# Optimization experiments

Hardware: AMD Instinct MI355X
Metric: run time of the kernel (lower is better)

Reference implementation:

```python
import jax, jax.numpy as jnp
import numpy as np

T, B, S = 2000, 64, 128   # seq_len, batch, alphabet_len
W = 16                    # beam_width
BLANK = 0                 # blank_index
PRUNE = 0.001             # prune_threshold
NONBLANK = np.array([c for c in range(S) if c != BLANK], dtype=np.int32)  # [S-1]
HASH_MULT = np.uint32(1000003)


def setup_inputs() -> dict:
    key = jax.random.key(0)
    k1, k2 = jax.random.split(key)
    x = jax.random.uniform(k1, (T, B, S), dtype=jnp.float32)
    lengths = jax.random.randint(k2, (B,), T // 2, T + 1, dtype=jnp.int32)
    return {"x": x, "lengths": lengths}


def _decode_one(ctc, length):
    # ctc: [T, S] probabilities for one utterance; length: scalar int32.
    nonblank = jnp.asarray(NONBLANK)
    arW = jnp.arange(W)

    prefixes0 = -jnp.ones((W, T), jnp.int32)          # padded prefixes
    len0 = jnp.zeros((W,), jnp.int32)
    # beam 0 = empty prefix (hash 0); others get unique sentinel hashes, prob 0
    hash0 = jnp.where(arW == 0, jnp.uint32(0),
                      jnp.uint32(0x80000000) + arW.astype(jnp.uint32))
    pb0 = jnp.zeros((W,), jnp.float32).at[0].set(1.0)  # Pb[-1][()] = 1
    pnb0 = jnp.zeros((W,), jnp.float32)                # Pnb[-1][()] = 0

    def step(carry, xs):
        prefixes, plen, h, p_b, p_nb = carry
        probs_raw, t = xs
        # pruning: symbols with prob <= threshold contribute nothing
        probs = jnp.where(probs_raw > PRUNE, probs_raw, 0.0)
        p_tot = p_b + p_nb
        last = jnp.where(plen > 0, prefixes[arW, jnp.maximum(plen - 1, 0)], -1)

        # --- candidates 0..W-1: prefix unchanged ---
        c0_pb = probs[BLANK] * p_tot                              # blank extends
        c0_pnb = jnp.where(last >= 0, probs[last] * p_nb, 0.0)    # repeat-last

        # --- candidates for beam b extended by nonblank symbol c: [W, S-1] ---
        pc = probs[nonblank]                                      # [S-1]
        rep = nonblank[None, :] == last[:, None]                  # [W, S-1]
        e_pnb = pc[None, :] * jnp.where(rep, p_b[:, None], p_tot[:, None])
        e_h = h[:, None] * HASH_MULT + (nonblank.astype(jnp.uint32) + 1)[None, :]
        e_pnb_f = e_pnb.reshape(-1)                               # [W*(S-1)]
        e_h_f = e_h.reshape(-1)

        # Merge: an extension can only coincide with another beam's unchanged
        # prefix (extensions of distinct prefixes are always distinct).
        eq = h[:, None] == e_h_f[None, :]                         # [W, W*(S-1)]
        u_pnb = c0_pnb + eq.astype(jnp.float32) @ e_pnb_f
        u_pb = c0_pb
        dup = eq.any(axis=0)

        key = jnp.concatenate([u_pb + u_pnb, jnp.where(dup, -1.0, e_pnb_f)])
        cand_pb = jnp.concatenate([u_pb, jnp.zeros_like(e_pnb_f)])
        cand_pnb = jnp.concatenate([u_pnb, jnp.where(dup, 0.0, e_pnb_f)])
        cand_h = jnp.concatenate([h, e_h_f])
        _, idx = jax.lax.top_k(key, W)

        ext = idx >= W
        q = jnp.maximum(idx - W, 0)
        nb = jnp.where(ext, q // (S - 1), idx)                    # source beam
        csym = jnp.where(ext, nonblank[q % (S - 1)], -1)          # appended sym
        base_pref = prefixes[nb]
        base_len = plen[nb]
        pos = jnp.arange(T)[None, :]
        n_pref = jnp.where((csym[:, None] >= 0) & (pos == base_len[:, None]),
                           csym[:, None], base_pref)
        n_len = base_len + (csym >= 0).astype(jnp.int32)
        n_h = cand_h[idx]
        n_pb = cand_pb[idx]
        n_pnb = cand_pnb[idx]

        # rescale to avoid fp underflow over long sequences (ranking-preserving;
        # the torch module returns only the argmax prefix, not raw scores)
        scale = 1.0 / jnp.maximum(jnp.max(n_pb + n_pnb), 1e-30)
        n_pb = n_pb * scale
        n_pnb = n_pnb * scale

        valid = t < length
        new = (n_pref, n_len, n_h, n_pb, n_pnb)
        old = (prefixes, plen, h, p_b, p_nb)
        carry = tuple(jnp.where(valid, a, b) for a, b in zip(new, old))
        return carry, None

    carry, _ = jax.lax.scan(jax.checkpoint(step),
                            (prefixes0, len0, hash0, pb0, pnb0),
                            (ctc, jnp.arange(T, dtype=jnp.int32)))
    prefixes, plen, _, p_b, p_nb = carry
    # top_k already sorted beams descending by total prob -> beam 0 is best
    return prefixes[0], plen[0], p_b[0] + p_nb[0]


def reference(x, lengths):
    # x: [T, B, S]; lengths: [B] int32
    prefs, lens, scores = jax.vmap(_decode_one, in_axes=(1, 0))(x, lengths)
    # prefs: [B, T] best prefix per element, padded with -1; lens: [B]
    return prefs, lens, scores
```

## Files before the change

kernel.cpp:

```cpp
#include <hip/hip_runtime.h>
#include <stdint.h>

#define T_ 2000
#define B_ 64
#define S_ 128
#define HASHM 1000003u

typedef float f4 __attribute__((ext_vector_type(4)));
typedef int i2v __attribute__((ext_vector_type(2)));

#if defined(__has_builtin)
#if __has_builtin(__builtin_amdgcn_permlane32_swap)
#define HAVE_PL32 1
#endif
#if __has_builtin(__builtin_amdgcn_permlane16_swap)
#define HAVE_PL16 1
#endif
#endif

__device__ __forceinline__ uint32_t rl(uint32_t v, int ln) {
  return (uint32_t)__builtin_amdgcn_readlane((int)v, ln);
}
__device__ __forceinline__ float rlf(float v, int ln) {
  return __uint_as_float(rl(__float_as_uint(v), ln));
}

__device__ __forceinline__ uint32_t fkey(float v) {
  uint32_t b = __float_as_uint(v);
  return b ^ (((int32_t)b < 0) ? 0xFFFFFFFFu : 0x80000000u);
}

__device__ __forceinline__ void wave_lds_fence() {
  asm volatile("s_waitcnt lgkmcnt(0)" ::: "memory");
}

template<int J>
__device__ __forceinline__ uint32_t bfly_u32(uint32_t v) {
  if constexpr (J == 1)
    return (uint32_t)__builtin_amdgcn_update_dpp((int)v, (int)v, 0xB1, 0xF, 0xF, false);
  else if constexpr (J == 2)
    return (uint32_t)__builtin_amdgcn_update_dpp((int)v, (int)v, 0x4E, 0xF, 0xF, false);
  else if constexpr (J == 4) {
    uint32_t a = (uint32_t)__builtin_amdgcn_update_dpp((int)v, (int)v, 0x12C, 0xF, 0xF, false);
    uint32_t b = (uint32_t)__builtin_amdgcn_update_dpp((int)v, (int)v, 0x124, 0xF, 0xF, false);
    return ((threadIdx.x & 4) == 0) ? a : b;
  } else if constexpr (J == 8)
    return (uint32_t)__builtin_amdgcn_update_dpp((int)v, (int)v, 0x128, 0xF, 0xF, false);
  else if constexpr (J == 16) {
#ifdef HAVE_PL16
    i2v r = __builtin_amdgcn_permlane16_swap((int)v, (int)v, false, false);
    return (uint32_t)(((threadIdx.x & 16) == 0) ? r[1] : r[0]);
#else
    return (uint32_t)__builtin_amdgcn_ds_swizzle((int)v, 0x401F);
#endif
  } else {
#ifdef HAVE_PL32
    i2v r = __builtin_amdgcn_permlane32_swap((int)v, (int)v, false, false);
    return (uint32_t)(((threadIdx.x & 32) == 0) ? r[1] : r[0]);
#else
    return (uint32_t)__shfl_xor((int)v, 32);
#endif
  }
}
template<int J>
__device__ __forceinline__ uint64_t bfly_u64(uint64_t v) {
  uint32_t lo = bfly_u32<J>((uint32_t)v);
  uint32_t hi = bfly_u32<J>((uint32_t)(v >> 32));
  return ((uint64_t)hi << 32) | lo;
}

#define BSTF(KK, J) { float p_ = __uint_as_float(bfly_u32<J>(__float_as_uint(v))); \
  bool d_ = ((ln & (KK)) == 0) == ((ln & (J)) == 0); \
  float mx_ = fmaxf(v, p_), mn_ = fminf(v, p_); v = d_ ? mx_ : mn_; }
#define BST64(KK, J) { uint64_t p_ = bfly_u64<J>(v); \
  bool d_ = ((ln & (KK)) == 0) == ((ln & (J)) == 0); \
  uint64_t mx_ = v > p_ ? v : p_, mn_ = v > p_ ? p_ : v; v = d_ ? mx_ : mn_; }

__device__ __forceinline__ float bsort64_f32(float v, const int ln) {
  BSTF(2, 1)
  BSTF(4, 2) BSTF(4, 1)
  BSTF(8, 4) BSTF(8, 2) BSTF(8, 1)
  BSTF(16, 8) BSTF(16, 4) BSTF(16, 2) BSTF(16, 1)
  BSTF(32, 16) BSTF(32, 8) BSTF(32, 4) BSTF(32, 2) BSTF(32, 1)
  BSTF(64, 32) BSTF(64, 16) BSTF(64, 8) BSTF(64, 4) BSTF(64, 2) BSTF(64, 1)
  return v;
}

template<int WIDTH>
__device__ __forceinline__ uint64_t bsortN_u64(uint64_t v, const int ln) {
  BST64(2, 1)
  BST64(4, 2) BST64(4, 1)
  BST64(8, 4) BST64(8, 2) BST64(8, 1)
  BST64(16, 8) BST64(16, 4) BST64(16, 2) BST64(16, 1)
  if constexpr (WIDTH >= 32) {
    BST64(32, 16) BST64(32, 8) BST64(32, 4) BST64(32, 2) BST64(32, 1)
  }
  if constexpr (WIDTH >= 64) {
    BST64(64, 32) BST64(64, 16) BST64(64, 8) BST64(64, 4) BST64(64, 2) BST64(64, 1)
  }
  return v;
}

__device__ __forceinline__ uint32_t incl_scan_add(uint32_t v) {
  v += (uint32_t)__builtin_amdgcn_update_dpp(0, (int)v, 0x111, 0xF, 0xF, false);
  v += (uint32_t)__builtin_amdgcn_update_dpp(0, (int)v, 0x112, 0xF, 0xF, false);
  v += (uint32_t)__builtin_amdgcn_update_dpp(0, (int)v, 0x114, 0xF, 0xF, false);
  v += (uint32_t)__builtin_amdgcn_update_dpp(0, (int)v, 0x118, 0xF, 0xF, false);
  v += (uint32_t)__builtin_amdgcn_update_dpp(0, (int)v, 0x142, 0xA, 0xF, false);
  v += (uint32_t)__builtin_amdgcn_update_dpp(0, (int)v, 0x143, 0xC, 0xF, false);
  return v;
}

template<int CTRL>
__device__ __forceinline__ uint64_t dpp_max_u64(uint64_t v) {
  uint32_t lo = (uint32_t)v, hi = (uint32_t)(v >> 32);
  uint32_t slo = (uint32_t)__builtin_amdgcn_update_dpp(0, (int)lo, CTRL, 0xF, 0xF, false);
  uint32_t shi = (uint32_t)__builtin_amdgcn_update_dpp(0, (int)hi, CTRL, 0xF, 0xF, false);
  uint64_t o = ((uint64_t)shi << 32) | slo;
  return (o > v) ? o : v;
}
__device__ __forceinline__ uint64_t wave_max_u64(uint64_t v) {
  v = dpp_max_u64<0x111>(v);
  v = dpp_max_u64<0x112>(v);
  v = dpp_max_u64<0x114>(v);
  v = dpp_max_u64<0x118>(v);
  v = dpp_max_u64<0x142>(v);
  v = dpp_max_u64<0x143>(v);
  uint32_t lo = rl((uint32_t)v, 63);
  uint32_t hi = rl((uint32_t)(v >> 32), 63);
  return ((uint64_t)hi << 32) | lo;
}

__global__ __launch_bounds__(64, 1) void ctc_decode_kernel(
    const float* __restrict__ x, const int* __restrict__ lengths,
    float* __restrict__ out) {
  __shared__ uint64_t surv[64];
  __shared__ __align__(16) float Pr[2][S_];
  __shared__ __align__(8) uint16_t trace[T_ * 16];

  const int b = blockIdx.x;
  const int lane = (int)threadIdx.x;
  const int m = lane & 15;
  const int g = lane >> 4;
  const int lenb = lengths[b];

  uint32_t h = (m == 0) ? 0u : (0x80000000u + (uint32_t)m);
  float pb = (m == 0) ? 1.0f : 0.0f;
  float pnb = 0.0f;
  int last = -1;
  int len = 0;

  float cur0;
  {
    const float* xt = x + (size_t)b * S_;
    float a0 = xt[lane], a1 = xt[lane + 64];
    float p0 = (a0 > 0.001f) ? a0 : 0.0f;
    float p1 = (a1 > 0.001f) ? a1 : 0.0f;
    Pr[0][lane] = p0;
    Pr[0][lane + 64] = p1;
    cur0 = p0;
  }

  const uint32_t cbase = 1u + 32u * (uint32_t)g;
  const uint32_t nrefb = ~(15u + (uint32_t)m * 127u + 32u * (uint32_t)g);

  for (int t = 0; t < lenb; ++t) {
    const float* P = Pr[t & 1];
    float r0n = 0.0f, r1n = 0.0f;
    const bool hasNext = (t + 1 < lenb);
    if (hasNext) {
      const float* xt = x + ((size_t)(t + 1) * B_ + b) * S_;
      r0n = xt[lane];
      r1n = xt[lane + 64];
    }
    wave_lds_fence();
    const uint32_t hM = h * HASHM;
    const uint32_t hMc = hM + cbase;

    const float ptot = __fadd_rn(pb, pnb);
    const float P0 = rlf(cur0, 0);
    const float c0pb = __fmul_rn(P0, ptot);
    const float plast = P[(last >= 0) ? last : 0];
    const float c0pnb = (last >= 0) ? __fmul_rn(plast, pnb) : 0.0f;

    uint32_t lmask = 0;
    uint32_t matchcnt = 0, jm = 0, cc = 1;
    #pragma unroll
    for (int j = 0; j < 16; ++j) {
      uint32_t s_h = rl(h, j);
      uint32_t p = s_h - hMc;
      lmask |= (p < 32u) ? (1u << (p & 31u)) : 0u;
      uint32_t d = h - s_h * HASHM;
      bool match = (d - 2u) <= 126u;
      cc = match ? (d - 1u) : cc;
      jm = match ? (uint32_t)j : jm;
      matchcnt += match ? 1u : 0u;
    }

    float term0;
    if (__builtin_expect(__ballot(matchcnt > 1u) == 0ull, 1)) {
      float tpb = __shfl(pb, (int)jm);
      float tpt = __shfl(ptot, (int)jm);
      int tlast = __shfl(last, (int)jm);
      float tv = P[cc];
      float sel = ((int)cc == tlast) ? tpb : tpt;
      term0 = (matchcnt != 0u) ? __fmul_rn(tv, sel) : 0.0f;
    } else {
      float term[16];
      #pragma unroll
      for (int j = 0; j < 16; ++j) {
        uint32_t s_h = rl(h, j);
        uint32_t d = h - s_h * HASHM;
        bool match2 = (d - 2u) <= 126u;
        uint32_t cc2 = match2 ? (d - 1u) : 1u;
        float tv = P[cc2];
        uint32_t slst = rl((uint32_t)last, j);
        float sel = (cc2 == slst) ? rlf(pb, j) : rlf(ptot, j);
        term[j] = match2 ? __fmul_rn(tv, sel) : 0.0f;
      }
      #pragma unroll
      for (int st = 1; st < 16; st <<= 1) {
        #pragma unroll
        for (int i2 = 0; i2 < 16; i2 += 2 * st)
          term[i2] = __fadd_rn(term[i2], term[i2 + st]);
      }
      term0 = term[0];
    }
    const float upnb = __fadd_rn(c0pnb, term0);
    const float key16 = __fadd_rn(c0pb, upnb);

    f4 pv[8];
    {
      const f4* P4 = (const f4*)(P + 32 * g);
      #pragma unroll
      for (int i = 0; i < 8; ++i) pv[i] = P4[i];
    }
    const int lk = last - 32 * g;
    float kf[32];
    #pragma unroll
    for (int k = 0; k < 32; ++k) {
      float pc = pv[k >> 2][k & 3];
      float sel = (k == lk) ? pb : ptot;
      float val = __fmul_rn(pc, sel);
      bool dup = (lmask >> k) & 1u;
      float kv = dup ? -1.0f : val;
      if (k == 0) kv = (lane < 16) ? key16 : kv;
      kf[k] = kv;
    }

    float mx[16];
    #pragma unroll
    for (int i = 0; i < 16; ++i) mx[i] = fmaxf(kf[2 * i], kf[2 * i + 1]);
    #pragma unroll
    for (int w2 = 8; w2 >= 1; w2 >>= 1) {
      #pragma unroll
      for (int i = 0; i < w2; ++i) mx[i] = fmaxf(mx[i], mx[i + w2]);
    }
    const float m1 = mx[0];

    float th = rlf(bsort64_f32(m1, lane), 15);

    uint32_t gcnt[4];
    #pragma unroll
    for (int grp = 0; grp < 4; ++grp) {
      uint32_t c2 = 0;
      #pragma unroll
      for (int k = grp * 8; k < grp * 8 + 8; ++k) c2 += (kf[k] >= th) ? 1u : 0u;
      gcnt[grp] = c2;
    }
    uint32_t cnt = (gcnt[0] + gcnt[1]) + (gcnt[2] + gcnt[3]);
    uint32_t incl = incl_scan_add(cnt);
    uint32_t M = rl(incl, 63);

    if (__builtin_expect(M > 64u, 0)) {
      float t1[16], t2[16];
      #pragma unroll
      for (int i = 0; i < 16; ++i) {
        float a2 = kf[2 * i], b2 = kf[2 * i + 1];
        t1[i] = fmaxf(a2, b2);
        t2[i] = fminf(a2, b2);
      }
      #pragma unroll
      for (int w2 = 8; w2 >= 1; w2 >>= 1) {
        #pragma unroll
        for (int i = 0; i < w2; ++i) {
          float A = t1[i], Bv = t1[i + w2];
          float sa = t2[i], sb = t2[i + w2];
          t1[i] = fmaxf(A, Bv);
          t2[i] = fmaxf(fminf(A, Bv), fmaxf(sa, sb));
        }
      }
      float th2 = rlf(bsort64_f32(t2[0], lane), 7);
      th = fmaxf(th, th2);
      #pragma unroll
      for (int grp = 0; grp < 4; ++grp) {
        uint32_t c2 = 0;
        #pragma unroll
        for (int k = grp * 8; k < grp * 8 + 8; ++k) c2 += (kf[k] >= th) ? 1u : 0u;
        gcnt[grp] = c2;
      }
      cnt = (gcnt[0] + gcnt[1]) + (gcnt[2] + gcnt[3]);
      incl = incl_scan_add(cnt);
      M = rl(incl, 63);
    }

    uint64_t selpk;
    if (__builtin_expect(M <= 64u, 1)) {
      uint64_t* dump = (uint64_t*)(&trace[(size_t)t * 16]);
      uint32_t base0 = incl - cnt;
      uint32_t base1 = base0 + gcnt[0];
      uint32_t base2 = base1 + gcnt[1];
      uint32_t base3 = base2 + gcnt[2];
      uint32_t bases[4] = {base0, base1, base2, base3};
      #pragma unroll
      for (int grp = 0; grp < 4; ++grp) {
        uint32_t pos = bases[grp];
        #pragma unroll
        for (int kk = 0; kk < 8; ++kk) {
          int k = grp * 8 + kk;
          bool q = kf[k] >= th;
          uint32_t nr = nrefb - (uint32_t)k;
          if (k == 0) nr = (lane < 16) ? ~(uint32_t)m : nr;
          uint64_t pk = ((uint64_t)__float_as_uint(kf[k]) << 32) | nr;
          uint64_t* dst = q ? &surv[pos] : dump;
          *dst = pk;
          pos += q ? 1u : 0u;
        }
      }
      wave_lds_fence();
      uint64_t w = ((uint32_t)lane < M) ? surv[lane] : 0ull;
      if (M <= 16u)      w = bsortN_u64<16>(w, lane);
      else if (M <= 32u) w = bsortN_u64<32>(w, lane);
      else               w = bsortN_u64<64>(w, lane);
      uint64_t s16 = bfly_u64<16>(w);
      uint64_t w01 = ((lane & 16) == 0) ? w : s16;
      uint64_t s32 = bfly_u64<32>(w01);
      selpk = ((lane & 32) == 0) ? w01 : s32;
    } else {
      uint32_t alive = 0xFFFFFFFFu;
      selpk = 0;
      #pragma unroll 1
      for (int r = 0; r < 16; ++r) {
        float bk = -1.0f;
        uint32_t bi = 0;
        #pragma unroll
        for (int k = 0; k < 32; ++k) {
          float kv = ((alive >> k) & 1u) ? kf[k] : -1.0f;
          if (kv > bk) { bk = kv; bi = (uint32_t)k; }
        }
        uint32_t nr = nrefb - bi;
        nr = (bi == 0u && lane < 16) ? ~(uint32_t)m : nr;
        uint64_t cand = ((uint64_t)fkey(bk) << 32) | nr;
        uint64_t win = wave_max_u64(cand);
        if (cand == win) alive &= ~(1u << bi);
        if (r == m) selpk = win;
      }
      uint32_t kb = (uint32_t)(selpk >> 32);
      kb ^= ((int32_t)kb < 0) ? 0x80000000u : 0xFFFFFFFFu;
      selpk = ((uint64_t)kb << 32) | (uint32_t)selpk;
    }

    if (hasNext) {
      float p0 = (r0n > 0.001f) ? r0n : 0.0f;
      float p1 = (r1n > 0.001f) ? r1n : 0.0f;
      float* Pn = Pr[(t + 1) & 1];
      Pn[lane] = p0;
      Pn[lane + 64] = p1;
      cur0 = p0;
    }

    const uint32_t gref = ~((uint32_t)selpk);
    const uint32_t keyw = (uint32_t)(selpk >> 32);
    const bool unch = gref < 16u;
    const uint32_t qq = gref - 16u;
    const uint32_t bsrc = qq / 127u;
    const uint32_t jj = qq - bsrc * 127u;
    const uint32_t c = jj + 1u;
    const int srcl = unch ? (int)gref : (int)bsrc;

    const uint32_t s_h = (uint32_t)__shfl((int)h, srcl);
    const uint32_t lpack = ((uint32_t)(last + 1) & 0xFFu) | ((uint32_t)len << 8);
    const uint32_t s_lp = (uint32_t)__shfl((int)lpack, srcl);
    const float s_upb = __shfl(c0pb, srcl);
    const float s_upn = __shfl(upnb, srcl);
    const int s_lst = (int)(s_lp & 0xFFu) - 1;
    const int s_len = (int)(s_lp >> 8);

    const uint32_t n_h = unch ? s_h : (s_h * HASHM + (jj + 2u));
    const float n_pb = unch ? s_upb : 0.0f;
    const float n_pnb = unch ? s_upn : __uint_as_float(keyw);
    const int n_last = unch ? s_lst : (int)c;
    const int n_len = unch ? s_len : (s_len + 1);

    if (lane < 16) {
      trace[t * 16 + lane] =
          (uint16_t)(((uint32_t)srcl << 8) | (unch ? 0u : c));
    }

    const float mxf = fmaxf(__uint_as_float(rl(keyw, 0)), 1e-30f);
    const float scale = __fdiv_rn(1.0f, mxf);
    pb = __fmul_rn(n_pb, scale);
    pnb = __fmul_rn(n_pnb, scale);
    h = n_h; last = n_last; len = n_len;
  }

  __syncthreads();

  float* prefs = out;
  float* lensOut = out + (B_ * T_);
  float* scores = out + (B_ * T_) + B_;

  const int L0 = __shfl(len, 0);
  for (int i = L0 + lane; i < T_; i += 64) prefs[(size_t)b * T_ + i] = -1.0f;

  if (lane == 0) {
    lensOut[b] = (float)L0;
    scores[b] = __fadd_rn(pb, pnb);
    int w = 0;
    int pos2 = L0 - 1;
    for (int t2 = lenb - 1; t2 >= 0; --t2) {
      uint32_t rec = trace[t2 * 16 + w];
      uint32_t sym = rec & 0xFFu;
      if (sym) { prefs[(size_t)b * T_ + pos2] = (float)sym; --pos2; }
      w = (int)(rec >> 8);
    }
  }
}

extern "C" void kernel_launch(void* const* d_in, const int* in_sizes, int n_in,
                              void* d_out, int out_size, void* d_ws, size_t ws_size,
                              hipStream_t stream) {
  (void)in_sizes; (void)n_in; (void)d_ws; (void)ws_size; (void)out_size;
  const float* x = (const float*)d_in[0];
  const int* lengths = (const int*)d_in[1];
  float* out = (float*)d_out;
  ctc_decode_kernel<<<B_, 64, 0, stream>>>(x, lengths, out);
}
```

Before: 7.241 ms.

## Shorten per-step critical path: single LDS buffer, no fences, reorder scoring

Drops the explicit LDS waitcnt fences and the double-buffered probability array, relying on in-order LDS access within a single wave. The unchanged-prefix merge term is moved after the threshold sort, and the rescale factor is taken from the sorted maximum earlier so it leaves the dependency chain. Candidate IDs now use a 128 stride, so divide-by-127 becomes shift/mask. The 64-bit bitonic compares use double fmax/fmin instead of integer compares. The risks are that removing the fences permits LDS reordering hazards, and that the double comparison misorders keys whose bit patterns are not valid ordered doubles.

After: 7.550 ms. 1.04x slower.

```diff
diff --git a/kernel.cpp b/kernel.cpp
--- a/kernel.cpp
+++ b/kernel.cpp
@@ -28,10 +28,6 @@
 __device__ __forceinline__ uint32_t fkey(float v) {
   uint32_t b = __float_as_uint(v);
   return b ^ (((int32_t)b < 0) ? 0xFFFFFFFFu : 0x80000000u);
-}
-
-__device__ __forceinline__ void wave_lds_fence() {
-  asm volatile("s_waitcnt lgkmcnt(0)" ::: "memory");
 }
 
 template<int J>
@@ -72,9 +68,13 @@
 #define BSTF(KK, J) { float p_ = __uint_as_float(bfly_u32<J>(__float_as_uint(v))); \
   bool d_ = ((ln & (KK)) == 0) == ((ln & (J)) == 0); \
   float mx_ = fmaxf(v, p_), mn_ = fminf(v, p_); v = d_ ? mx_ : mn_; }
+
 #define BST64(KK, J) { uint64_t p_ = bfly_u64<J>(v); \
   bool d_ = ((ln & (KK)) == 0) == ((ln & (J)) == 0); \
-  uint64_t mx_ = v > p_ ? v : p_, mn_ = v > p_ ? p_ : v; v = d_ ? mx_ : mn_; }
+  double vd_ = __longlong_as_double((long long)v); \
+  double pd_ = __longlong_as_double((long long)p_); \
+  double mx_ = fmax(vd_, pd_), mn_ = fmin(vd_, pd_); \
+  v = (uint64_t)__double_as_longlong(d_ ? mx_ : mn_); }
 
 __device__ __forceinline__ float bsort64_f32(float v, const int ln) {
   BSTF(2, 1)
@@ -135,7 +135,7 @@
     const float* __restrict__ x, const int* __restrict__ lengths,
     float* __restrict__ out) {
   __shared__ uint64_t surv[64];
-  __shared__ __align__(16) float Pr[2][S_];
+  __shared__ __align__(16) float Pr[S_];
   __shared__ __align__(8) uint16_t trace[T_ * 16];
 
   const int b = blockIdx.x;
@@ -156,16 +156,16 @@
     float a0 = xt[lane], a1 = xt[lane + 64];
     float p0 = (a0 > 0.001f) ? a0 : 0.0f;
     float p1 = (a1 > 0.001f) ? a1 : 0.0f;
-    Pr[0][lane] = p0;
-    Pr[0][lane + 64] = p1;
+    Pr[lane] = p0;
+    Pr[lane + 64] = p1;
     cur0 = p0;
   }
 
   const uint32_t cbase = 1u + 32u * (uint32_t)g;
-  const uint32_t nrefb = ~(15u + (uint32_t)m * 127u + 32u * (uint32_t)g);
+  const uint32_t nrefb = ~(15u + ((uint32_t)m << 7) + 32u * (uint32_t)g);
 
   for (int t = 0; t < lenb; ++t) {
-    const float* P = Pr[t & 1];
+    const float* P = Pr;
     float r0n = 0.0f, r1n = 0.0f;
     const bool hasNext = (t + 1 < lenb);
     if (hasNext) {
@@ -173,7 +173,6 @@
       r0n = xt[lane];
       r1n = xt[lane + 64];
     }
-    wave_lds_fence();
     const uint32_t hM = h * HASHM;
     const uint32_t hMc = hM + cbase;
 
@@ -181,7 +180,13 @@
     const float P0 = rlf(cur0, 0);
     const float c0pb = __fmul_rn(P0, ptot);
     const float plast = P[(last >= 0) ? last : 0];
-    const float c0pnb = (last >= 0) ? __fmul_rn(plast, pnb) : 0.0f;
+
+    f4 pv[8];
+    {
+      const f4* P4 = (const f4*)(P + 32 * g);
+      #pragma unroll
+      for (int i = 0; i < 8; ++i) pv[i] = P4[i];
+    }
 
     uint32_t lmask = 0;
     uint32_t matchcnt = 0, jm = 0, cc = 1;
@@ -196,45 +201,13 @@
       jm = match ? (uint32_t)j : jm;
       matchcnt += match ? 1u : 0u;
     }
-
-    float term0;
-    if (__builtin_expect(__ballot(matchcnt > 1u) == 0ull, 1)) {
-      float tpb = __shfl(pb, (int)jm);
-      float tpt = __shfl(ptot, (int)jm);
-      int tlast = __shfl(last, (int)jm);
-      float tv = P[cc];
-      float sel = ((int)cc == tlast) ? tpb : tpt;
-      term0 = (matchcnt != 0u) ? __fmul_rn(tv, sel) : 0.0f;
-    } else {
-      float term[16];
-      #pragma unroll
-      for (int j = 0; j < 16; ++j) {
-        uint32_t s_h = rl(h, j);
-        uint32_t d = h - s_h * HASHM;
-        bool match2 = (d - 2u) <= 126u;
-        uint32_t cc2 = match2 ? (d - 1u) : 1u;
-        float tv = P[cc2];
-        uint32_t slst = rl((uint32_t)last, j);
-        float sel = (cc2 == slst) ? rlf(pb, j) : rlf(ptot, j);
-        term[j] = match2 ? __fmul_rn(tv, sel) : 0.0f;
-      }
-      #pragma unroll
-      for (int st = 1; st < 16; st <<= 1) {
-        #pragma unroll
-        for (int i2 = 0; i2 < 16; i2 += 2 * st)
-          term[i2] = __fadd_rn(term[i2], term[i2 + st]);
-      }
-      term0 = term[0];
-    }
-    const float upnb = __fadd_rn(c0pnb, term0);
-    const float key16 = __fadd_rn(c0pb, upnb);
-
-    f4 pv[8];
-    {
-      const f4* P4 = (const f4*)(P + 32 * g);
-      #pragma unroll
-      for (int i = 0; i < 8; ++i) pv[i] = P4[i];
-    }
+    const bool multi = (__ballot(matchcnt > 1u) != 0ull);
+
+    float tv = P[cc];
+    float tpb = __shfl(pb, (int)jm);
+    float tpt = __shfl(ptot, (int)jm);
+    int tlast = __shfl(last, (int)jm);
+
     const int lk = last - 32 * g;
     float kf[32];
     #pragma unroll
@@ -244,7 +217,7 @@
       float val = __fmul_rn(pc, sel);
       bool dup = (lmask >> k) & 1u;
       float kv = dup ? -1.0f : val;
-      if (k == 0) kv = (lane < 16) ? key16 : kv;
+      if (k == 0) kv = (lane < 16) ? c0pb : kv;
       kf[k] = kv;
     }
 
@@ -256,9 +229,38 @@
       #pragma unroll
       for (int i = 0; i < w2; ++i) mx[i] = fmaxf(mx[i], mx[i + w2]);
     }
-    const float m1 = mx[0];
-
-    float th = rlf(bsort64_f32(m1, lane), 15);
+
+    float th = rlf(bsort64_f32(mx[0], lane), 15);
+
+    const float c0pnb = (last >= 0) ? __fmul_rn(plast, pnb) : 0.0f;
+    float term0;
+    if (__builtin_expect(!multi, 1)) {
+      float sel = ((int)cc == tlast) ? tpb : tpt;
+      term0 = (matchcnt != 0u) ? __fmul_rn(tv, sel) : 0.0f;
+    } else {
+      float term[16];
+      #pragma unroll
+      for (int j = 0; j < 16; ++j) {
+        uint32_t s_h = rl(h, j);
+        uint32_t d = h - s_h * HASHM;
+        bool match2 = (d - 2u) <= 126u;
+        uint32_t cc2 = match2 ? (d - 1u) : 1u;
+        float tv2 = P[cc2];
+        uint32_t slst = rl((uint32_t)last, j);
+        float sel = (cc2 == slst) ? rlf(pb, j) : rlf(ptot, j);
+        term[j] = match2 ? __fmul_rn(tv2, sel) : 0.0f;
+      }
+      #pragma unroll
+      for (int st = 1; st < 16; st <<= 1) {
+        #pragma unroll
+        for (int i2 = 0; i2 < 16; i2 += 2 * st)
+          term[i2] = __fadd_rn(term[i2], term[i2 + st]);
+      }
+      term0 = term[0];
+    }
+    const float upnb = __fadd_rn(c0pnb, term0);
+    const float key16 = __fadd_rn(c0pb, upnb);
+    kf[0] = (lane < 16) ? key16 : kf[0];
 
     uint32_t gcnt[4];
     #pragma unroll
@@ -305,6 +307,7 @@
     }
 
     uint64_t selpk;
+    uint32_t k0raw;
     if (__builtin_expect(M <= 64u, 1)) {
       uint64_t* dump = (uint64_t*)(&trace[(size_t)t * 16]);
       uint32_t base0 = incl - cnt;
@@ -327,17 +330,18 @@
           pos += q ? 1u : 0u;
         }
       }
-      wave_lds_fence();
       uint64_t w = ((uint32_t)lane < M) ? surv[lane] : 0ull;
       if (M <= 16u)      w = bsortN_u64<16>(w, lane);
       else if (M <= 32u) w = bsortN_u64<32>(w, lane);
       else               w = bsortN_u64<64>(w, lane);
+      k0raw = rl((uint32_t)(w >> 32), 0);
       uint64_t s16 = bfly_u64<16>(w);
       uint64_t w01 = ((lane & 16) == 0) ? w : s16;
       uint64_t s32 = bfly_u64<32>(w01);
       selpk = ((lane & 32) == 0) ? w01 : s32;
     } else {
       uint32_t alive = 0xFFFFFFFFu;
+      uint32_t k0fk = 0;
       selpk = 0;
       #pragma unroll 1
       for (int r = 0; r < 16; ++r) {
@@ -354,18 +358,22 @@
         uint64_t win = wave_max_u64(cand);
         if (cand == win) alive &= ~(1u << bi);
         if (r == m) selpk = win;
+        if (r == 0) k0fk = (uint32_t)(win >> 32);
       }
       uint32_t kb = (uint32_t)(selpk >> 32);
       kb ^= ((int32_t)kb < 0) ? 0x80000000u : 0xFFFFFFFFu;
       selpk = ((uint64_t)kb << 32) | (uint32_t)selpk;
-    }
+      k0raw = k0fk ^ (((int32_t)k0fk < 0) ? 0x80000000u : 0xFFFFFFFFu);
+    }
+
+    const float mxf = fmaxf(__uint_as_float(k0raw), 1e-30f);
+    const float scale = __fdiv_rn(1.0f, mxf);
 
     if (hasNext) {
       float p0 = (r0n > 0.001f) ? r0n : 0.0f;
       float p1 = (r1n > 0.001f) ? r1n : 0.0f;
-      float* Pn = Pr[(t + 1) & 1];
-      Pn[lane] = p0;
-      Pn[lane + 64] = p1;
+      Pr[lane] = p0;
+      Pr[lane + 64] = p1;
       cur0 = p0;
     }
 
@@ -373,8 +381,8 @@
     const uint32_t keyw = (uint32_t)(selpk >> 32);
     const bool unch = gref < 16u;
     const uint32_t qq = gref - 16u;
-    const uint32_t bsrc = qq / 127u;
-    const uint32_t jj = qq - bsrc * 127u;
+    const uint32_t bsrc = qq >> 7;
+    const uint32_t jj = qq & 127u;
     const uint32_t c = jj + 1u;
     const int srcl = unch ? (int)gref : (int)bsrc;
 
@@ -397,8 +405,6 @@
           (uint16_t)(((uint32_t)srcl << 8) | (unch ? 0u : c));
     }
 
-    const float mxf = fmaxf(__uint_as_float(rl(keyw, 0)), 1e-30f);
-    const float scale = __fdiv_rn(1.0f, mxf);
     pb = __fmul_rn(n_pb, scale);
     pnb = __fmul_rn(n_pnb, scale);
     h = n_h; last = n_last; len = n_len;
```
